# Kernel optimization log

Measured on AMD Instinct MI355X. Metric: run time of the kernel, lower is better.

## Reference

```python
import jax, jax.numpy as jnp
import numpy as np

THRESHOLD = 0.5
DECAY = 0.95


def setup_inputs() -> dict:
    key = jax.random.key(0)
    x = jax.random.normal(key, (64, 1024, 512), dtype=jnp.float32)
    return {"x": x}


def reference(x):
    # x: [batch, seq_len, features]
    m0 = jnp.zeros(x[:, 0, :].shape, dtype=x.dtype)  # membrane potential [B, F]

    def step(m, xt):
        m = DECAY * m + xt                      # leaky integrate
        s = (m > THRESHOLD).astype(x.dtype)     # fire
        m = m * (1.0 - s)                       # reset fired neurons
        return m, s

    # scan over time (leading axis)
    _, spikes = jax.lax.scan(step, m0, jnp.swapaxes(x, 0, 1))  # [S, B, F]
    return jnp.swapaxes(spikes, 0, 1)  # [B, S, F]
```

## Files before the change

kernel.cpp:

```cpp
#include <hip/hip_runtime.h>


#define BATCH 64
#define SEQ   1024
#define FEAT  512
#define UNROLL 16

__global__ __launch_bounds__(64, 1)
void lif_kernel(const float* __restrict__ x, float* __restrict__ out) {
    const int tid = blockIdx.x * blockDim.x + threadIdx.x;
    const int b = tid >> 9;
    const int f = tid & (FEAT - 1);
    const size_t base = (size_t)b * SEQ * FEAT + f;
    const float* __restrict__ xp = x + base;
    float* __restrict__ op = out + base;

    float m = 0.0f;
    float cur[UNROLL], nxt[UNROLL];

#pragma unroll
    for (int u = 0; u < UNROLL; ++u) cur[u] = xp[(size_t)u * FEAT];

    for (int t0 = 0; t0 < SEQ; t0 += UNROLL) {
        if (t0 + UNROLL < SEQ) {
            const float* __restrict__ xn = xp + (size_t)(t0 + UNROLL) * FEAT;
#pragma unroll
            for (int u = 0; u < UNROLL; ++u) nxt[u] = xn[(size_t)u * FEAT];
        }

#pragma unroll
        for (int u = 0; u < UNROLL; ++u) {
            m = __fadd_rn(__fmul_rn(0.95f, m), cur[u]);
            const bool fired = (m > 0.5f);
            op[(size_t)(t0 + u) * FEAT] = fired ? 1.0f : 0.0f;
            m = fired ? 0.0f : m;
        }

#pragma unroll
        for (int u = 0; u < UNROLL; ++u) cur[u] = nxt[u];
    }
}

extern "C" void kernel_launch(void* const* d_in, const int* in_sizes, int n_in,
                              void* d_out, int out_size, void* d_ws, size_t ws_size,
                              hipStream_t stream) {
    const float* x = (const float*)d_in[0];
    float* out = (float*)d_out;
    const int total_threads = BATCH * FEAT;
    const int block = 64;
    const int grid = total_threads / block;
    lif_kernel<<<grid, block, 0, stream>>>(x, out);
}
```

Baseline: 56.63 us.

## Stage input chunks via async global-to-LDS loads and vectorize spike stores

Replaces the per-thread strided register prefetch with double-buffered 64-step chunks that are loaded straight into LDS using global_load_lds with 16-byte transfers per lane. The spikes for each chunk are written to LDS and then stored to global memory as 128-bit nontemporal vector stores. Manual vmcnt/lgkmcnt waits and sched barriers order the pipeline. The aim is fewer, wider memory transactions and load latency hidden behind the serial recurrence, at the cost of extra LDS traffic and fragile hand-tuned wait counts.

```diff
diff --git a/kernel.cpp b/kernel.cpp
--- a/kernel.cpp
+++ b/kernel.cpp
@@ -4,41 +4,76 @@
 #define BATCH 64
 #define SEQ   1024
 #define FEAT  512
-#define UNROLL 16
+#define CHUNK 64
+#define NCHUNK (SEQ / CHUNK)
+#define LPC 16
+
+typedef const __attribute__((address_space(1))) void gas_void;
+typedef __attribute__((address_space(3))) void las_void;
+typedef float f32x4 __attribute__((ext_vector_type(4)));
 
 __global__ __launch_bounds__(64, 1)
 void lif_kernel(const float* __restrict__ x, float* __restrict__ out) {
-    const int tid = blockIdx.x * blockDim.x + threadIdx.x;
-    const int b = tid >> 9;
-    const int f = tid & (FEAT - 1);
-    const size_t base = (size_t)b * SEQ * FEAT + f;
-    const float* __restrict__ xp = x + base;
-    float* __restrict__ op = out + base;
+    __shared__ float lds_x[2][CHUNK * 64];
+    __shared__ float lds_s[CHUNK * 64];
+
+    const int bid  = blockIdx.x;
+    const int b    = bid >> 3;
+    const int f0   = (bid & 7) << 6;
+    const int lane = threadIdx.x;
+
+    const int t_sub = lane >> 4;
+    const int fw    = (lane & 15) << 2;
+
+    const float* __restrict__ xp = x   + (size_t)b * SEQ * FEAT + f0;
+    float* __restrict__       op = out + (size_t)b * SEQ * FEAT + f0;
+
+#define STAGE(bufidx, t0)                                                     \
+    {                                                                         \
+        _Pragma("unroll")                                                     \
+        for (int i = 0; i < LPC; ++i) {                                       \
+            const float* src = xp + (size_t)((t0) + 4 * i + t_sub) * FEAT + fw; \
+            __builtin_amdgcn_global_load_lds(                                 \
+                (gas_void*)src, (las_void*)&lds_x[bufidx][i * 256], 16, 0, 0); \
+        }                                                                     \
+    }
 
     float m = 0.0f;
-    float cur[UNROLL], nxt[UNROLL];
+
+    STAGE(0, 0)
+
+    for (int k = 0; k < NCHUNK; ++k) {
+        const int buf = k & 1;
+        if (k + 1 < NCHUNK) STAGE(buf ^ 1, (k + 1) * CHUNK)
+
+        if (k == 0 || k == NCHUNK - 1)
+            asm volatile("s_waitcnt vmcnt(16)" ::: "memory");
+        else
+            asm volatile("s_waitcnt vmcnt(32)" ::: "memory");
+        __builtin_amdgcn_sched_barrier(0);
 
 #pragma unroll
-    for (int u = 0; u < UNROLL; ++u) cur[u] = xp[(size_t)u * FEAT];
-
-    for (int t0 = 0; t0 < SEQ; t0 += UNROLL) {
-        if (t0 + UNROLL < SEQ) {
-            const float* __restrict__ xn = xp + (size_t)(t0 + UNROLL) * FEAT;
-#pragma unroll
-            for (int u = 0; u < UNROLL; ++u) nxt[u] = xn[(size_t)u * FEAT];
-        }
-
-#pragma unroll
-        for (int u = 0; u < UNROLL; ++u) {
-            m = __fadd_rn(__fmul_rn(0.95f, m), cur[u]);
+        for (int t = 0; t < CHUNK; ++t) {
+            const float xv = lds_x[buf][t * 64 + lane];
+            m = __fadd_rn(__fmul_rn(0.95f, m), xv);
             const bool fired = (m > 0.5f);
-            op[(size_t)(t0 + u) * FEAT] = fired ? 1.0f : 0.0f;
+            lds_s[t * 64 + lane] = fired ? 1.0f : 0.0f;
             m = fired ? 0.0f : m;
         }
 
+        asm volatile("s_waitcnt lgkmcnt(0)" ::: "memory");
+        __builtin_amdgcn_sched_barrier(0);
+
+        const int t0 = k * CHUNK;
 #pragma unroll
-        for (int u = 0; u < UNROLL; ++u) cur[u] = nxt[u];
+        for (int i = 0; i < LPC; ++i) {
+            const f32x4 v =
+                *reinterpret_cast<const f32x4*>(&lds_s[i * 256 + 4 * lane]);
+            __builtin_nontemporal_store(
+                v, reinterpret_cast<f32x4*>(op + (size_t)(t0 + 4 * i + t_sub) * FEAT + fw));
+        }
     }
+#undef STAGE
 }
 
 extern "C" void kernel_launch(void* const* d_in, const int* in_sizes, int n_in,
@@ -46,8 +81,6 @@
                               hipStream_t stream) {
     const float* x = (const float*)d_in[0];
     float* out = (float*)d_out;
-    const int total_threads = BATCH * FEAT;
-    const int block = 64;
-    const int grid = total_threads / block;
-    lif_kernel<<<grid, block, 0, stream>>>(x, out);
+    const int grid = BATCH * 8;
+    lif_kernel<<<grid, 64, 0, stream>>>(x, out);
 }
```

Measured after the change: 49.39 us. 1.15x faster.
